# Kernel tuning notes

Measured on AMD Instinct MI355X. Metric: run time of the kernel, lower is better.

## Reference

```python
import jax, jax.numpy as jnp
import numpy as np

B, C, H, W = 8, 512, 64, 64
D = C // 8  # 64

def setup_inputs() -> dict:
    key = jax.random.key(0)
    ks = jax.random.split(key, 10)
    s = 0.02
    return {
        "x":  jax.random.normal(ks[0], (B, C, H, W), dtype=jnp.float32),
        "Wq": jax.random.normal(ks[1], (D, C), dtype=jnp.float32) * s,
        "bq": jnp.zeros((D,), dtype=jnp.float32),
        "Wk": jax.random.normal(ks[2], (D, C), dtype=jnp.float32) * s,
        "bk": jnp.zeros((D,), dtype=jnp.float32),
        "Wv": jax.random.normal(ks[3], (D, C), dtype=jnp.float32) * s,
        "bv": jnp.zeros((D,), dtype=jnp.float32),
        "Wo": jax.random.normal(ks[4], (C, D), dtype=jnp.float32) * s,
        "bo": jnp.zeros((C,), dtype=jnp.float32),
        "gamma": jnp.full((1,), 0.5, dtype=jnp.float32),
    }

def reference(x, Wq, bq, Wk, bk, Wv, bv, Wo, bo, gamma):
    b, c, h, w = x.shape
    n = h * w
    xf = x.reshape(b, c, n)                                   # (B, C, N)
    # 1x1 convs == channel matmuls (spectral_norm only reparametrizes the weight)
    q = jnp.einsum('dc,bcn->bnd', Wq, xf) + bq                # (B, N, D)
    k = jnp.einsum('dc,bcn->bdn', Wk, xf) + bk[:, None]       # (B, D, N)
    v = jnp.einsum('dc,bcn->bdn', Wv, xf) + bv[:, None]       # (B, D, N)
    # unscaled scores, softmax over key index (last dim)
    attn = jax.nn.softmax(jnp.einsum('bnd,bdm->bnm', q, k), axis=-1)  # (B, N, N)
    out = jnp.einsum('bdm,bnm->bdn', v, attn)                 # (B, D, N)
    out = jnp.einsum('cd,bdn->bcn', Wo, out) + bo[:, None]    # (B, C, N)
    return (out * gamma + xf).reshape(b, c, h, w)
```

## Files before the change

### kernel.cpp

```cpp
#include <hip/hip_runtime.h>
#include <hip/hip_bf16.h>

#define DEVFN __device__ __forceinline__

typedef __bf16 bf16x8 __attribute__((ext_vector_type(8)));
typedef float f32x4 __attribute__((ext_vector_type(4)));
typedef float float4_t __attribute__((ext_vector_type(4)));
typedef unsigned short ushort8_t __attribute__((ext_vector_type(8)));
typedef unsigned short ushort4_t __attribute__((ext_vector_type(4)));
typedef unsigned int uint4_t __attribute__((ext_vector_type(4)));

constexpr int Bd = 8, Cd = 512, Nd = 4096, Dd = 64;

DEVFN unsigned short f2bf(float f) {
    union { float f; unsigned int u; } v; v.f = f;
    unsigned int r = (v.u + 0x7FFFu + ((v.u >> 16) & 1u)) >> 16;
    return (unsigned short)r;
}

DEVFN unsigned int pack2(float a, float b) {
    __hip_bfloat162 h = __float22bfloat162_rn(make_float2(a, b));
    union { __hip_bfloat162 h; unsigned int u; } c; c.h = h;
    return c.u;
}

DEVFN bf16x8 ld_bf8(const unsigned short* p) {
    ushort8_t u = *(const ushort8_t*)p;
    return __builtin_bit_cast(bf16x8, u);
}

DEVFN f32x4 mfma16(bf16x8 a, bf16x8 b, f32x4 c) {
    return __builtin_amdgcn_mfma_f32_16x16x32_bf16(a, b, c, 0, 0, 0);
}

__global__ __launch_bounds__(256) void k_cvtw(
    const float* __restrict__ Wq, const float* __restrict__ Wk,
    const float* __restrict__ Wv, const float* __restrict__ Wo,
    unsigned short* __restrict__ w4)
{
    int i = blockIdx.x * 256 + threadIdx.x;
    w4[i]          = f2bf(Wq[i]);
    w4[32768 + i]  = f2bf(Wk[i]);
    w4[65536 + i]  = f2bf(Wv[i]);
    w4[98304 + i]  = f2bf(Wo[i]);
}

__global__ __launch_bounds__(64, 2) void k_qkv(
    const float* __restrict__ x,
    const unsigned short* __restrict__ w4,
    const float* __restrict__ bq, const float* __restrict__ bk, const float* __restrict__ bv,
    unsigned short* __restrict__ q_nd, unsigned short* __restrict__ k_nd,
    unsigned short* __restrict__ v_dn)
{
    const int n0w = blockIdx.x * 16;
    const int b   = blockIdx.y;
    const int l   = threadIdx.x, lo = l & 15, hi = l >> 4;
    const float* xb = x + (size_t)b * Cd * Nd + n0w;

    __shared__ __align__(16) unsigned short sm[64 * 24];

    f32x4 acc[12] = {};
    float4_t xsA[4], xsB[4];

    auto gloadA = [&](int t) {
        const float* p = xb + (size_t)(t * 64 + l) * Nd;
        #pragma unroll
        for (int i = 0; i < 4; ++i) xsA[i] = *(const float4_t*)(p + i * 4);
    };
    auto gloadB = [&](int t) {
        const float* p = xb + (size_t)(t * 64 + l) * Nd;
        #pragma unroll
        for (int i = 0; i < 4; ++i) xsB[i] = *(const float4_t*)(p + i * 4);
    };
    auto dswriteA = [&]() {
        #pragma unroll
        for (int i = 0; i < 16; ++i)
            sm[i * 72 + l] = f2bf(xsA[i >> 2][i & 3]);
    };
    auto dswriteB = [&]() {
        #pragma unroll
        for (int i = 0; i < 16; ++i)
            sm[i * 72 + l] = f2bf(xsB[i >> 2][i & 3]);
    };
    auto compute = [&](int t) {
        #pragma unroll
        for (int kk = 0; kk < 2; ++kk) {
            bf16x8 af = ld_bf8(&sm[lo * 72 + kk * 32 + hi * 8]);
            #pragma unroll
            for (int j = 0; j < 12; ++j) {
                const unsigned short* wm = w4 + (j >> 2) * 32768;
                bf16x8 bf = ld_bf8(wm + ((j & 3) * 16 + lo) * Cd + t * 64 + kk * 32 + hi * 8);
                acc[j] = mfma16(af, bf, acc[j]);
            }
        }
    };

    gloadA(0);
    gloadB(1);
    for (int t = 0; t < 8; t += 2) {
        dswriteA();
        asm volatile("" ::: "memory");
        if (t + 2 < 8) gloadA(t + 2);
        __builtin_amdgcn_sched_barrier(0);
        compute(t);
        asm volatile("" ::: "memory");
        dswriteB();
        asm volatile("" ::: "memory");
        if (t + 3 < 8) gloadB(t + 3);
        __builtin_amdgcn_sched_barrier(0);
        compute(t + 1);
        asm volatile("" ::: "memory");
    }

    #pragma unroll
    for (int m = 0; m < 2; ++m) {
        const float* bias = m ? bk : bq;
        #pragma unroll
        for (int j = 0; j < 4; ++j) {
            const float bia = bias[j * 16 + lo];
            #pragma unroll
            for (int r = 0; r < 4; ++r)
                sm[(hi * 4 + r) * 72 + j * 16 + lo] = f2bf(acc[m * 4 + j][r] + bia);
        }
        asm volatile("" ::: "memory");
        const int row = l >> 2, dg = l & 3;
        ushort8_t a0 = *(const ushort8_t*)&sm[row * 72 + dg * 16];
        ushort8_t a1 = *(const ushort8_t*)&sm[row * 72 + dg * 16 + 8];
        unsigned short* dst = (m ? k_nd : q_nd)
            + ((size_t)b * Nd + n0w + row) * 64 + dg * 16;
        *(ushort8_t*)dst = a0; *(ushort8_t*)(dst + 8) = a1;
        asm volatile("" ::: "memory");
    }

    #pragma unroll
    for (int j = 0; j < 4; ++j) {
        const float bia = bv[j * 16 + lo];
        #pragma unroll
        for (int r = 0; r < 4; ++r)
            sm[(j * 16 + lo) * 24 + hi * 4 + r] = f2bf(acc[8 + j][r] + bia);
    }
    asm volatile("" ::: "memory");
    {
        ushort8_t a0 = *(const ushort8_t*)&sm[l * 24];
        ushort8_t a1 = *(const ushort8_t*)&sm[l * 24 + 8];
        unsigned short* dst = v_dn + ((size_t)b * Dd + l) * Nd + n0w;
        *(ushort8_t*)dst = a0; *(ushort8_t*)(dst + 8) = a1;
    }
}

__global__ __launch_bounds__(256, 4) void k_attn(
    const unsigned short* __restrict__ q_nd,
    const unsigned short* __restrict__ k_nd,
    const unsigned short* __restrict__ v_dn,
    unsigned short* __restrict__ o_nd)
{
    const int bid = blockIdx.x;
    const int b   = bid & 7;
    const int n0  = (bid >> 3) * 32;
    const int tid = threadIdx.x, wid = tid >> 6, l = tid & 63;
    const int lo  = l & 15, hi = l >> 4;
    const int lsw = lo & 7;
    const int qh  = wid >> 1;
    const int kh  = wid & 1;
    const int wk0 = kh * 32;

    __shared__ unsigned short k_tiles[2][64 * 64];
    __shared__ unsigned short v_tiles[2][64 * 64];
    float* red_acc = (float*)&k_tiles[0][0];
    float* red_l   = (float*)&v_tiles[0][0];

    const unsigned short* qb = q_nd + (size_t)b * Nd * Dd;
    const unsigned short* kb = k_nd + (size_t)b * Nd * Dd;
    const unsigned short* vb = v_dn + (size_t)b * Dd * Nd;

    bf16x8 aq[2];
    #pragma unroll
    for (int kc = 0; kc < 2; ++kc)
        aq[kc] = ld_bf8(qb + (size_t)(n0 + qh*16 + lo) * 64 + kc*32 + hi*8);

    f32x4 acc[4] = {};
    float l_p = 0.f;

    const int sr = tid >> 3, ss = tid & 7;
    const int kwsl = (ss ^ (sr & 7)) * 8;
    const int vkh = ss >> 2, vsl = ss & 3, vms = vsl >> 1;
    const int vg0 = vkh * 4 + ((2 * vsl) & 3);
    const int vg1 = vkh * 4 + ((2 * vsl + 1) & 3);
    const int vsw = sr & 7;
    ushort8_t kr0, kr1, vr0, vr1;

    auto gload = [&](int t) {
        const size_t m1 = (size_t)t * 64;
        kr0 = *(const ushort8_t*)(kb + (m1 + sr) * 64 + ss * 8);
        kr1 = *(const ushort8_t*)(kb + (m1 + 32 + sr) * 64 + ss * 8);
        vr0 = *(const ushort8_t*)(vb + (size_t)sr * Nd + m1 + ss * 8);
        vr1 = *(const ushort8_t*)(vb + (size_t)(32 + sr) * Nd + m1 + ss * 8);
    };
    auto dswrite = [&](int buf) {
        unsigned short* kt = k_tiles[buf];
        unsigned short* vt = v_tiles[buf];
        *(ushort8_t*)(kt + sr * 64 + kwsl)        = kr0;
        *(ushort8_t*)(kt + (32 + sr) * 64 + kwsl) = kr1;
        ushort4_t a0 = __builtin_shufflevector(vr0, vr0, 0, 1, 2, 3);
        ushort4_t a1 = __builtin_shufflevector(vr0, vr0, 4, 5, 6, 7);
        ushort4_t b0 = __builtin_shufflevector(vr1, vr1, 0, 1, 2, 3);
        ushort4_t b1 = __builtin_shufflevector(vr1, vr1, 4, 5, 6, 7);
        *(ushort4_t*)(vt + sr * 64 + (vg0 ^ vsw) * 8 + vms * 4)        = a0;
        *(ushort4_t*)(vt + sr * 64 + (vg1 ^ vsw) * 8 + vms * 4)        = a1;
        *(ushort4_t*)(vt + (32 + sr) * 64 + (vg0 ^ vsw) * 8 + vms * 4) = b0;
        *(ushort4_t*)(vt + (32 + sr) * 64 + (vg1 ^ vsw) * 8 + vms * 4) = b1;
    };

    auto compute = [&](int buf) {
        const unsigned short* kt = k_tiles[buf];
        const unsigned short* vt = v_tiles[buf];
        f32x4 s[2] = {};
        #pragma unroll
        for (int ms = 0; ms < 2; ++ms) {
            #pragma unroll
            for (int kc = 0; kc < 2; ++kc) {
                bf16x8 kf = ld_bf8(kt + (wk0 + ms*16 + lo) * 64 + (((kc*4 + hi) ^ lsw) * 8));
                s[ms] = mfma16(kf, aq[kc], s[ms]);
            }
        }
        bf16x8 vf[4];
        #pragma unroll
        for (int ds = 0; ds < 4; ++ds)
            vf[ds] = ld_bf8(vt + (ds*16 + lo) * 64 + (((kh*4 + hi) ^ lsw) * 8));
        float p[2][4];
        #pragma unroll
        for (int ms = 0; ms < 2; ++ms)
            #pragma unroll
            for (int r = 0; r < 4; ++r)
                p[ms][r] = __expf(s[ms][r]);
        l_p += ((p[0][0] + p[0][1]) + (p[0][2] + p[0][3]))
             + ((p[1][0] + p[1][1]) + (p[1][2] + p[1][3]));
        uint4_t w;
        w[0] = pack2(p[0][0], p[0][1]);
        w[1] = pack2(p[0][2], p[0][3]);
        w[2] = pack2(p[1][0], p[1][1]);
        w[3] = pack2(p[1][2], p[1][3]);
        bf16x8 apf = __builtin_bit_cast(bf16x8, w);
        #pragma unroll
        for (int ds = 0; ds < 4; ++ds)
            acc[ds] = mfma16(apf, vf[ds], acc[ds]);
    };

    constexpr int NT = Nd / 64;
    gload(0);
    dswrite(0);
    __syncthreads();
    for (int t = 0; t < NT; ++t) {
        const int cur = t & 1;
        if (t + 1 < NT) gload(t + 1);
        __builtin_amdgcn_sched_barrier(0);
        compute(cur);
        if (t + 1 < NT) dswrite(cur ^ 1);
        __syncthreads();
    }

    float lh = l_p;
    lh += __shfl_xor(lh, 16, 64);
    lh += __shfl_xor(lh, 32, 64);
    if (kh == 1) {
        #pragma unroll
        for (int ds = 0; ds < 4; ++ds)
            *(f32x4*)&red_acc[(qh * 4 + ds) * 256 + l * 4] = acc[ds];
        red_l[qh * 16 + lo] = lh;
    }
    __syncthreads();
    if (kh == 0) {
        #pragma unroll
        for (int ds = 0; ds < 4; ++ds)
            acc[ds] += *(const f32x4*)&red_acc[(qh * 4 + ds) * 256 + l * 4];
        float l_tot = lh + red_l[qh * 16 + lo];
        #pragma unroll
        for (int r = 0; r < 4; ++r) {
            float lq = __shfl(l_tot, hi * 4 + r, 16);
            float rl = 1.0f / lq;
            #pragma unroll
            for (int ds = 0; ds < 4; ++ds) {
                float o = acc[ds][r] * rl;
                o_nd[((size_t)b * Nd + n0 + qh*16 + hi*4 + r) * 64 + ds*16 + lo] = f2bf(o);
            }
        }
    }
}

__global__ __launch_bounds__(256) void k_oproj(
    const unsigned short* __restrict__ o_nd,
    const unsigned short* __restrict__ wo,
    const float* __restrict__ bo,
    const float* __restrict__ gamma,
    const float* __restrict__ x,
    float* __restrict__ out)
{
    const int b   = blockIdx.y;
    const int n0  = blockIdx.x * 64;
    const int tid = threadIdx.x, wid = tid >> 6, l = tid & 63;
    const int lo  = l & 15, hi = l >> 4;
    const int n0w = n0 + wid * 16;
    const float g = gamma[0];

    bf16x8 ao[2];
    #pragma unroll
    for (int kc = 0; kc < 2; ++kc)
        ao[kc] = ld_bf8(o_nd + ((size_t)b * Nd + n0w + lo) * 64 + kc*32 + hi*8);

    for (int ct = 0; ct < 32; ++ct) {
        f32x4 acc = {};
        #pragma unroll
        for (int kc = 0; kc < 2; ++kc) {
            bf16x8 bw = ld_bf8(wo + (ct*16 + lo) * 64 + kc*32 + hi*8);
            acc = mfma16(ao[kc], bw, acc);
        }
        const int c = ct*16 + lo;
        const float bc = bo[c];
        const size_t base = ((size_t)b * Cd + c) * Nd + n0w + hi*4;
        float4_t xv = *(const float4_t*)(x + base);
        float4_t ov;
        #pragma unroll
        for (int r = 0; r < 4; ++r) ov[r] = g * (acc[r] + bc) + xv[r];
        *(float4_t*)(out + base) = ov;
    }
}

extern "C" void kernel_launch(void* const* d_in, const int* in_sizes, int n_in,
                              void* d_out, int out_size, void* d_ws, size_t ws_size,
                              hipStream_t stream) {
    (void)in_sizes; (void)n_in; (void)out_size; (void)ws_size;
    const float* x  = (const float*)d_in[0];
    const float* Wq = (const float*)d_in[1];
    const float* bq = (const float*)d_in[2];
    const float* Wk = (const float*)d_in[3];
    const float* bk = (const float*)d_in[4];
    const float* Wv = (const float*)d_in[5];
    const float* bv = (const float*)d_in[6];
    const float* Wo = (const float*)d_in[7];
    const float* bo = (const float*)d_in[8];
    const float* gm = (const float*)d_in[9];
    float* out = (float*)d_out;

    unsigned short* w4   = (unsigned short*)d_ws;
    unsigned short* q_nd = w4 + 131072;
    unsigned short* k_nd = q_nd + (size_t)Bd * Nd * Dd;
    unsigned short* v_dn = k_nd + (size_t)Bd * Nd * Dd;
    unsigned short* o_nd = v_dn + (size_t)Bd * Nd * Dd;

    k_cvtw<<<128, 256, 0, stream>>>(Wq, Wk, Wv, Wo, w4);
    dim3 gq(Nd / 16, Bd);
    k_qkv<<<gq, 64, 0, stream>>>(x, w4, bq, bk, bv, q_nd, k_nd, v_dn);
    k_attn<<<1024, 256, 0, stream>>>(q_nd, k_nd, v_dn, o_nd);
    dim3 g1(Nd / 64, Bd);
    k_oproj<<<g1, 256, 0, stream>>>(o_nd, w4 + 98304, bo, gm, x, out);
}
```

Baseline: 166.5 us.

## Split QKV channel reduction across two waves; double query rows per attention block

Result: slower. 193.8 us (+16.4%).

```diff
diff --git a/kernel.cpp b/kernel.cpp
--- a/kernel.cpp
+++ b/kernel.cpp
@@ -45,7 +45,7 @@
     w4[98304 + i]  = f2bf(Wo[i]);
 }
 
-__global__ __launch_bounds__(64, 2) void k_qkv(
+__global__ __launch_bounds__(128, 4) void k_qkv(
     const float* __restrict__ x,
     const unsigned short* __restrict__ w4,
     const float* __restrict__ bq, const float* __restrict__ bk, const float* __restrict__ bv,
@@ -54,21 +54,28 @@
 {
     const int n0w = blockIdx.x * 16;
     const int b   = blockIdx.y;
-    const int l   = threadIdx.x, lo = l & 15, hi = l >> 4;
+    const int tid = threadIdx.x;
+    const int w   = tid >> 6;
+    const int l   = tid & 63, lo = l & 15, hi = l >> 4;
+    const int cb  = w * 256;
     const float* xb = x + (size_t)b * Cd * Nd + n0w;
 
-    __shared__ __align__(16) unsigned short sm[64 * 24];
+    __shared__ __align__(16) unsigned short stg[2][16 * 72];
+    __shared__ __align__(16) float red[12][64][4];
+    __shared__ __align__(16) unsigned short epi[64 * 24];
+
+    unsigned short* sm = &stg[w][0];
 
     f32x4 acc[12] = {};
     float4_t xsA[4], xsB[4];
 
     auto gloadA = [&](int t) {
-        const float* p = xb + (size_t)(t * 64 + l) * Nd;
+        const float* p = xb + (size_t)(cb + t * 64 + l) * Nd;
         #pragma unroll
         for (int i = 0; i < 4; ++i) xsA[i] = *(const float4_t*)(p + i * 4);
     };
     auto gloadB = [&](int t) {
-        const float* p = xb + (size_t)(t * 64 + l) * Nd;
+        const float* p = xb + (size_t)(cb + t * 64 + l) * Nd;
         #pragma unroll
         for (int i = 0; i < 4; ++i) xsB[i] = *(const float4_t*)(p + i * 4);
     };
@@ -89,7 +96,7 @@
             #pragma unroll
             for (int j = 0; j < 12; ++j) {
                 const unsigned short* wm = w4 + (j >> 2) * 32768;
-                bf16x8 bf = ld_bf8(wm + ((j & 3) * 16 + lo) * Cd + t * 64 + kk * 32 + hi * 8);
+                bf16x8 bf = ld_bf8(wm + ((j & 3) * 16 + lo) * Cd + cb + t * 64 + kk * 32 + hi * 8);
                 acc[j] = mfma16(af, bf, acc[j]);
             }
         }
@@ -97,21 +104,33 @@
 
     gloadA(0);
     gloadB(1);
-    for (int t = 0; t < 8; t += 2) {
+    for (int t = 0; t < 4; t += 2) {
         dswriteA();
         asm volatile("" ::: "memory");
-        if (t + 2 < 8) gloadA(t + 2);
+        if (t + 2 < 4) gloadA(t + 2);
         __builtin_amdgcn_sched_barrier(0);
         compute(t);
         asm volatile("" ::: "memory");
         dswriteB();
         asm volatile("" ::: "memory");
-        if (t + 3 < 8) gloadB(t + 3);
+        if (t + 3 < 4) gloadB(t + 3);
         __builtin_amdgcn_sched_barrier(0);
         compute(t + 1);
         asm volatile("" ::: "memory");
     }
 
+    if (w == 1) {
+        #pragma unroll
+        for (int j = 0; j < 12; ++j)
+            *(f32x4*)&red[j][l][0] = acc[j];
+    }
+    __syncthreads();
+    if (w == 1) return;
+
+    #pragma unroll
+    for (int j = 0; j < 12; ++j)
+        acc[j] += *(const f32x4*)&red[j][l][0];
+
     #pragma unroll
     for (int m = 0; m < 2; ++m) {
         const float* bias = m ? bk : bq;
@@ -120,12 +139,12 @@
             const float bia = bias[j * 16 + lo];
             #pragma unroll
             for (int r = 0; r < 4; ++r)
-                sm[(hi * 4 + r) * 72 + j * 16 + lo] = f2bf(acc[m * 4 + j][r] + bia);
+                epi[(hi * 4 + r) * 72 + j * 16 + lo] = f2bf(acc[m * 4 + j][r] + bia);
         }
         asm volatile("" ::: "memory");
         const int row = l >> 2, dg = l & 3;
-        ushort8_t a0 = *(const ushort8_t*)&sm[row * 72 + dg * 16];
-        ushort8_t a1 = *(const ushort8_t*)&sm[row * 72 + dg * 16 + 8];
+        ushort8_t a0 = *(const ushort8_t*)&epi[row * 72 + dg * 16];
+        ushort8_t a1 = *(const ushort8_t*)&epi[row * 72 + dg * 16 + 8];
         unsigned short* dst = (m ? k_nd : q_nd)
             + ((size_t)b * Nd + n0w + row) * 64 + dg * 16;
         *(ushort8_t*)dst = a0; *(ushort8_t*)(dst + 8) = a1;
@@ -137,18 +156,18 @@
         const float bia = bv[j * 16 + lo];
         #pragma unroll
         for (int r = 0; r < 4; ++r)
-            sm[(j * 16 + lo) * 24 + hi * 4 + r] = f2bf(acc[8 + j][r] + bia);
+            epi[(j * 16 + lo) * 24 + hi * 4 + r] = f2bf(acc[8 + j][r] + bia);
     }
     asm volatile("" ::: "memory");
     {
-        ushort8_t a0 = *(const ushort8_t*)&sm[l * 24];
-        ushort8_t a1 = *(const ushort8_t*)&sm[l * 24 + 8];
+        ushort8_t a0 = *(const ushort8_t*)&epi[l * 24];
+        ushort8_t a1 = *(const ushort8_t*)&epi[l * 24 + 8];
         unsigned short* dst = v_dn + ((size_t)b * Dd + l) * Nd + n0w;
         *(ushort8_t*)dst = a0; *(ushort8_t*)(dst + 8) = a1;
     }
 }
 
-__global__ __launch_bounds__(256, 4) void k_attn(
+__global__ __launch_bounds__(256, 2) void k_attn(
     const unsigned short* __restrict__ q_nd,
     const unsigned short* __restrict__ k_nd,
     const unsigned short* __restrict__ v_dn,
@@ -156,7 +175,7 @@
 {
     const int bid = blockIdx.x;
     const int b   = bid & 7;
-    const int n0  = (bid >> 3) * 32;
+    const int n0  = (bid >> 3) * 64;
     const int tid = threadIdx.x, wid = tid >> 6, l = tid & 63;
     const int lo  = l & 15, hi = l >> 4;
     const int lsw = lo & 7;
@@ -166,20 +185,22 @@
 
     __shared__ unsigned short k_tiles[2][64 * 64];
     __shared__ unsigned short v_tiles[2][64 * 64];
-    float* red_acc = (float*)&k_tiles[0][0];
-    float* red_l   = (float*)&v_tiles[0][0];
+    __shared__ float red_acc[2][2][4][256];
+    __shared__ float red_l[2][2][16];
 
     const unsigned short* qb = q_nd + (size_t)b * Nd * Dd;
     const unsigned short* kb = k_nd + (size_t)b * Nd * Dd;
     const unsigned short* vb = v_dn + (size_t)b * Dd * Nd;
 
-    bf16x8 aq[2];
-    #pragma unroll
-    for (int kc = 0; kc < 2; ++kc)
-        aq[kc] = ld_bf8(qb + (size_t)(n0 + qh*16 + lo) * 64 + kc*32 + hi*8);
-
-    f32x4 acc[4] = {};
-    float l_p = 0.f;
+    bf16x8 aq[2][2];
+    #pragma unroll
+    for (int qs = 0; qs < 2; ++qs)
+        #pragma unroll
+        for (int kc = 0; kc < 2; ++kc)
+            aq[qs][kc] = ld_bf8(qb + (size_t)(n0 + qh*32 + qs*16 + lo) * 64 + kc*32 + hi*8);
+
+    f32x4 acc[2][4] = {};
+    float l_p[2] = {0.f, 0.f};
 
     const int sr = tid >> 3, ss = tid & 7;
     const int kwsl = (ss ^ (sr & 7)) * 8;
@@ -214,36 +235,41 @@
     auto compute = [&](int buf) {
         const unsigned short* kt = k_tiles[buf];
         const unsigned short* vt = v_tiles[buf];
-        f32x4 s[2] = {};
+        f32x4 s[2][2] = {};
         #pragma unroll
         for (int ms = 0; ms < 2; ++ms) {
             #pragma unroll
             for (int kc = 0; kc < 2; ++kc) {
                 bf16x8 kf = ld_bf8(kt + (wk0 + ms*16 + lo) * 64 + (((kc*4 + hi) ^ lsw) * 8));
-                s[ms] = mfma16(kf, aq[kc], s[ms]);
+                #pragma unroll
+                for (int qs = 0; qs < 2; ++qs)
+                    s[qs][ms] = mfma16(kf, aq[qs][kc], s[qs][ms]);
             }
         }
         bf16x8 vf[4];
         #pragma unroll
         for (int ds = 0; ds < 4; ++ds)
             vf[ds] = ld_bf8(vt + (ds*16 + lo) * 64 + (((kh*4 + hi) ^ lsw) * 8));
-        float p[2][4];
-        #pragma unroll
-        for (int ms = 0; ms < 2; ++ms)
-            #pragma unroll
-            for (int r = 0; r < 4; ++r)
-                p[ms][r] = __expf(s[ms][r]);
-        l_p += ((p[0][0] + p[0][1]) + (p[0][2] + p[0][3]))
-             + ((p[1][0] + p[1][1]) + (p[1][2] + p[1][3]));
-        uint4_t w;
-        w[0] = pack2(p[0][0], p[0][1]);
-        w[1] = pack2(p[0][2], p[0][3]);
-        w[2] = pack2(p[1][0], p[1][1]);
-        w[3] = pack2(p[1][2], p[1][3]);
-        bf16x8 apf = __builtin_bit_cast(bf16x8, w);
-        #pragma unroll
-        for (int ds = 0; ds < 4; ++ds)
-            acc[ds] = mfma16(apf, vf[ds], acc[ds]);
+        #pragma unroll
+        for (int qs = 0; qs < 2; ++qs) {
+            float p[2][4];
+            #pragma unroll
+            for (int ms = 0; ms < 2; ++ms)
+                #pragma unroll
+                for (int r = 0; r < 4; ++r)
+                    p[ms][r] = __expf(s[qs][ms][r]);
+            l_p[qs] += ((p[0][0] + p[0][1]) + (p[0][2] + p[0][3]))
+                     + ((p[1][0] + p[1][1]) + (p[1][2] + p[1][3]));
+            uint4_t w;
+            w[0] = pack2(p[0][0], p[0][1]);
+            w[1] = pack2(p[0][2], p[0][3]);
+            w[2] = pack2(p[1][0], p[1][1]);
+            w[3] = pack2(p[1][2], p[1][3]);
+            bf16x8 apf = __builtin_bit_cast(bf16x8, w);
+            #pragma unroll
+            for (int ds = 0; ds < 4; ++ds)
+                acc[qs][ds] = mfma16(apf, vf[ds], acc[qs][ds]);
+        }
     };
 
     constexpr int NT = Nd / 64;
@@ -259,29 +285,40 @@
         __syncthreads();
     }
 
-    float lh = l_p;
-    lh += __shfl_xor(lh, 16, 64);
-    lh += __shfl_xor(lh, 32, 64);
+    float lh[2];
+    #pragma unroll
+    for (int qs = 0; qs < 2; ++qs) {
+        float ps = l_p[qs];
+        ps += __shfl_xor(ps, 16, 64);
+        ps += __shfl_xor(ps, 32, 64);
+        lh[qs] = ps;
+    }
     if (kh == 1) {
         #pragma unroll
-        for (int ds = 0; ds < 4; ++ds)
-            *(f32x4*)&red_acc[(qh * 4 + ds) * 256 + l * 4] = acc[ds];
-        red_l[qh * 16 + lo] = lh;
+        for (int qs = 0; qs < 2; ++qs) {
+            #pragma unroll
+            for (int ds = 0; ds < 4; ++ds)
+                *(f32x4*)&red_acc[qh][qs][ds][l * 4] = acc[qs][ds];
+            red_l[qh][qs][lo] = lh[qs];
+        }
     }
     __syncthreads();
     if (kh == 0) {
         #pragma unroll
-        for (int ds = 0; ds < 4; ++ds)
-            acc[ds] += *(const f32x4*)&red_acc[(qh * 4 + ds) * 256 + l * 4];
-        float l_tot = lh + red_l[qh * 16 + lo];
-        #pragma unroll
-        for (int r = 0; r < 4; ++r) {
-            float lq = __shfl(l_tot, hi * 4 + r, 16);
-            float rl = 1.0f / lq;
-            #pragma unroll
-            for (int ds = 0; ds < 4; ++ds) {
-                float o = acc[ds][r] * rl;
-                o_nd[((size_t)b * Nd + n0 + qh*16 + hi*4 + r) * 64 + ds*16 + lo] = f2bf(o);
+        for (int qs = 0; qs < 2; ++qs) {
+            #pragma unroll
+            for (int ds = 0; ds < 4; ++ds)
+                acc[qs][ds] += *(const f32x4*)&red_acc[qh][qs][ds][l * 4];
+            float l_tot = lh[qs] + red_l[qh][qs][lo];
+            #pragma unroll
+            for (int r = 0; r < 4; ++r) {
+                float lq = __shfl(l_tot, hi * 4 + r, 16);
+                float rl = 1.0f / lq;
+                #pragma unroll
+                for (int ds = 0; ds < 4; ++ds) {
+                    float o = acc[qs][ds][r] * rl;
+                    o_nd[((size_t)b * Nd + n0 + qh*32 + qs*16 + hi*4 + r) * 64 + ds*16 + lo] = f2bf(o);
+                }
             }
         }
     }
@@ -349,8 +386,8 @@
 
     k_cvtw<<<128, 256, 0, stream>>>(Wq, Wk, Wv, Wo, w4);
     dim3 gq(Nd / 16, Bd);
-    k_qkv<<<gq, 64, 0, stream>>>(x, w4, bq, bk, bv, q_nd, k_nd, v_dn);
-    k_attn<<<1024, 256, 0, stream>>>(q_nd, k_nd, v_dn, o_nd);
+    k_qkv<<<gq, 128, 0, stream>>>(x, w4, bq, bk, bv, q_nd, k_nd, v_dn);
+    k_attn<<<512, 256, 0, stream>>>(q_nd, k_nd, v_dn, o_nd);
     dim3 g1(Nd / 64, Bd);
     k_oproj<<<g1, 256, 0, stream>>>(o_nd, w4 + 98304, bo, gm, x, out);
 }
```
